# Kernel tuning notes

Measured on AMD Instinct MI355X. Metric: run time of the kernel, lower is better.

Reference implementation:

```python
import jax, jax.numpy as jnp
import numpy as np

N = 50000          # nodes
E = 800000         # edges (before self loops)
F_IN = 16
HID = 64
HEADS = 4
C = 64             # per-head out channels (concat=False)
G = 64             # graphs in batch
NEG_SLOPE = 0.2


def setup_inputs() -> dict:
    key = jax.random.key(0)
    ks = jax.random.split(key, 20)
    inp = {
        "x": jax.random.normal(ks[0], (N, F_IN), jnp.float32),
        "edge_index": jax.random.randint(ks[1], (2, E), 0, N, jnp.int64),
        "batch": jnp.sort(jax.random.randint(ks[2], (N,), 0, G, jnp.int64)),
        "W_in": jax.random.normal(ks[3], (HID, F_IN), jnp.float32) * 0.1,
        "b_in": jnp.zeros((HID,), jnp.float32),
        "W_out": jax.random.normal(ks[4], (1, HID), jnp.float32) * 0.1,
        "b_out": jnp.zeros((1,), jnp.float32),
    }
    for l in range(3):
        inp[f"W{l}"] = jax.random.normal(ks[5 + 4 * l], (HEADS * C, HID), jnp.float32) * 0.1
        inp[f"asrc{l}"] = jax.random.normal(ks[6 + 4 * l], (HEADS, C), jnp.float32) * 0.1
        inp[f"adst{l}"] = jax.random.normal(ks[7 + 4 * l], (HEADS, C), jnp.float32) * 0.1
        inp[f"bg{l}"] = jnp.zeros((HID,), jnp.float32)
    return inp


def _gat_layer(x, W, a_src, a_dst, bias, src, dst, n):
    # x: [N, HID] -> h: [N, HEADS, C]
    h = (x @ W.T).reshape(n, HEADS, C)
    alpha_s = jnp.einsum("nhc,hc->nh", h, a_src)   # [N, H]
    alpha_d = jnp.einsum("nhc,hc->nh", h, a_dst)
    e = jax.nn.leaky_relu(alpha_s[src] + alpha_d[dst], NEG_SLOPE)  # [E', H]
    # segment softmax over incoming edges of each dst node
    m = jax.ops.segment_max(e, dst, num_segments=n)
    e = jnp.exp(e - m[dst])
    s = jax.ops.segment_sum(e, dst, num_segments=n)
    alpha = e / (s[dst] + 1e-16)                                   # [E', H]
    msg = alpha[:, :, None] * h[src]                               # [E', H, C]
    out = jax.ops.segment_sum(msg, dst, num_segments=n)            # [N, H, C]
    return out.mean(axis=1) + bias                                 # concat=False: head mean


def reference(x, W_in, b_in, W0, asrc0, adst0, bg0, W1, asrc1, adst1, bg1,
              W2, asrc2, adst2, bg2, W_out, b_out, edge_index, batch):
    n = x.shape[0]
    # add self loops (PyG GATConv default)
    loops = jnp.arange(n, dtype=edge_index.dtype)
    src = jnp.concatenate([edge_index[0], loops])
    dst = jnp.concatenate([edge_index[1], loops])

    h = x @ W_in.T + b_in
    for W, a_s, a_d, bg in ((W0, asrc0, adst0, bg0),
                            (W1, asrc1, adst1, bg1),
                            (W2, asrc2, adst2, bg2)):
        h = jax.nn.relu(_gat_layer(h, W, a_s, a_d, bg, src, dst, n))
        # dropout p=0.2 is inactive in eval mode

    # global mean pool over graphs
    sums = jax.ops.segment_sum(h, batch, num_segments=G)
    cnt = jax.ops.segment_sum(jnp.ones((n,), h.dtype), batch, num_segments=G)
    graph_emb = sums / jnp.maximum(cnt, 1.0)[:, None]              # [G, HID]

    return jax.nn.sigmoid(graph_emb @ W_out.T + b_out)             # [G, 1]
```

## Files before the change

### kernel.cpp

```cpp
#include <hip/hip_runtime.h>
#include <hip/hip_bf16.h>
#include <hip/hip_fp16.h>

#define HID 64
#define HEADS 4
#define GCNT 64
#define F_IN 16
#define NEG 0.2f
#define NBUCK 256
#define BSLOT 6144
#define SCHUNK 2048

typedef _Float16 f16x8 __attribute__((ext_vector_type(8)));
typedef float f32x4 __attribute__((ext_vector_type(4)));

__device__ __forceinline__ unsigned pack_h2(float a, float b) {
  __half2 h = __floats2half2_rn(a, b);
  union { __half2 h; unsigned u; } c;
  c.h = h;
  return c.u;
}
__device__ __forceinline__ __half2 uas_h2(unsigned u) {
  union { unsigned u; __half2 h; } c;
  c.u = u;
  return c.h;
}
__device__ __forceinline__ unsigned h2_as_u(__half2 h) {
  union { __half2 h; unsigned u; } c;
  c.h = h;
  return c.u;
}
__device__ __forceinline__ __half2 xor16_add(__half2 v) {
  unsigned u = (unsigned)__shfl_xor((int)h2_as_u(v), 16, 64);
  return __hadd2(v, uas_h2(u));
}

__global__ __launch_bounds__(256) void k_pre(
    const float* __restrict__ W0, const float* __restrict__ asrc,
    const float* __restrict__ adst, int* __restrict__ bcur, float* __restrict__ va) {
  int t = threadIdx.x;
  if (blockIdx.x == 0) bcur[t] = 0;
  int idx = blockIdx.x * 256 + t;
  int q = idx >> 6, k = idx & 63;
  const float* a = (q < 4) ? asrc : adst;
  int h = q & 3;
  float s = 0.f;
  for (int c = 0; c < 64; ++c) s += a[h * 64 + c] * W0[(h * 64 + c) * 64 + k];
  va[idx] = s;
}

__global__ __launch_bounds__(256) void k_bucket(
    const int* __restrict__ ei, int* __restrict__ bcur,
    unsigned* __restrict__ tmp, int E, int N) {
  __shared__ int hist[NBUCK];
  __shared__ int base[NBUCK];
  int t = threadIdx.x;
  int start = blockIdx.x * SCHUNK;
  int end = min(start + SCHUNK, E + N);
  hist[t] = 0;
  __syncthreads();
  unsigned val[8];
  int rank[8];
  bool ok[8];
#pragma unroll
  for (int k = 0; k < 8; ++k) {
    int i = start + t + k * 256;
    ok[k] = i < end;
    if (ok[k]) {
      int s, d;
      if (i < E) {
        s = ei[i];
        d = ei[E + i];
      } else {
        s = d = i - E;
      }
      val[k] = ((unsigned)d << 16) | (unsigned)s;
      rank[k] = atomicAdd(&hist[d >> 8], 1);
    }
  }
  __syncthreads();
  int h = hist[t];
  base[t] = h ? atomicAdd(&bcur[t], h) : 0;
  __syncthreads();
#pragma unroll
  for (int k = 0; k < 8; ++k) {
    if (ok[k]) {
      int bk = (int)(val[k] >> 24);
      int idx = base[bk] + rank[k];
      if (idx < BSLOT) tmp[(size_t)bk * BSLOT + idx] = val[k];
    }
  }
}

__global__ __launch_bounds__(256) void k_bsort(
    const unsigned* __restrict__ tmp, const int* __restrict__ bcur,
    int* __restrict__ rowptr, int* __restrict__ col, int N) {
  __shared__ int s[NBUCK];
  __shared__ int hist[NBUCK];
  __shared__ int pref[NBUCK];
  int b = blockIdx.x, t = threadIdx.x;
  int c = min(bcur[t], BSLOT);
  s[t] = c;
  __syncthreads();
  for (int o = 1; o < 256; o <<= 1) {
    int x = (t >= o) ? s[t - o] : 0;
    __syncthreads();
    s[t] += x;
    __syncthreads();
  }
  int base = (b == 0) ? 0 : s[b - 1];
  int total = s[255];
  int cntb = min(bcur[b], BSLOT);
  hist[t] = 0;
  __syncthreads();
  for (int j = t; j < cntb; j += 256)
    atomicAdd(&hist[(tmp[(size_t)b * BSLOT + j] >> 16) & 255], 1);
  __syncthreads();
  int v = hist[t];
  pref[t] = v;
  __syncthreads();
  for (int o = 1; o < 256; o <<= 1) {
    int x = (t >= o) ? pref[t - o] : 0;
    __syncthreads();
    pref[t] += x;
    __syncthreads();
  }
  pref[t] -= v;
  __syncthreads();
  int node = b * 256 + t;
  if (node < N) rowptr[node] = base + pref[t];
  if (b == 255 && t == 255) rowptr[N] = total;
  hist[t] = 0;
  __syncthreads();
  for (int j = t; j < cntb; j += 256) {
    unsigned e = tmp[(size_t)b * BSLOT + j];
    int d8 = (int)((e >> 16) & 255);
    int r = atomicAdd(&hist[d8], 1);
    col[base + pref[d8] + r] = (int)(e & 0xffffu);
  }
}

__global__ void k_init(const float* __restrict__ x, const float* __restrict__ Win,
                       const float* __restrict__ bin,
                       const float* __restrict__ W0, const float* __restrict__ W1,
                       const float* __restrict__ W2,
                       __half* __restrict__ Wh3, __half* __restrict__ Wcat3,
                       float* __restrict__ sums, const float* __restrict__ va,
                       float* __restrict__ as_, float* __restrict__ ad_,
                       __half* __restrict__ hh, int N) {
  int b = blockIdx.x, t = threadIdx.x;
  if (b < 384) {
    int i = b * 256 + t;
    if (i < 49152) {
      const float* W = (i < 16384) ? W0 : (i < 32768) ? W1 : W2;
      Wh3[i] = __float2half(W[i & 16383]);
    } else {
      int j = i - 49152;
      int l = j >> 14;
      int r = j & 16383;
      int c = r >> 8;
      int k256 = r & 255;
      int h = k256 & 3, kk = k256 >> 2;
      const float* W = (l == 0) ? W0 : (l == 1) ? W1 : W2;
      Wcat3[j] = __float2half(0.25f * W[(h * 64 + c) * 64 + kk]);
    }
    return;
  }
  if (b < 401) {
    int i = (b - 384) * 256 + t;
    if (i < GCNT * HID + GCNT) sums[i] = 0.f;
    return;
  }
  int i = (b - 401) * 256 + t;
  if (i >= N * HID) return;
  int n = i >> 6, j = i & 63;
  const float* xr = x + (size_t)n * F_IN;
  const float* wr = Win + j * F_IN;
  float acc = bin[j];
#pragma unroll
  for (int k = 0; k < F_IN; ++k) acc += xr[k] * wr[k];
  hh[i] = __float2half(acc);
  float r[8];
#pragma unroll
  for (int q = 0; q < 8; ++q) {
    float v = acc * va[q * 64 + j];
#pragma unroll
    for (int o = 32; o; o >>= 1) v += __shfl_xor(v, o, 64);
    r[q] = v;
  }
  if (j == 0) {
    *(float4*)(as_ + (size_t)n * 4) = make_float4(r[0], r[1], r[2], r[3]);
    *(float4*)(ad_ + (size_t)n * 4) = make_float4(r[4], r[5], r[6], r[7]);
  }
}

__device__ __forceinline__ void gat_one_node(
    int node, int lane, const __half* __restrict__ h, const float* __restrict__ as_,
    const float* __restrict__ ad_, const int* __restrict__ rowptr,
    const int* __restrict__ col, __half* __restrict__ M, int N) {
  int r0 = rowptr[node];
  int deg = rowptr[node + 1] - r0;
  float4 adv = *(const float4*)(ad_ + (size_t)node * 4);

  if (deg <= 64) {
    int off = 0;
    float x0 = 0.f, x1 = 0.f, x2 = 0.f, x3 = 0.f;
    if (lane < deg) {
      int s = col[r0 + lane];
      off = s << 6;
      float4 av = *(const float4*)(as_ + (size_t)s * 4);
      float e0 = av.x + adv.x; e0 = (e0 > 0.f) ? e0 : NEG * e0;
      float e1 = av.y + adv.y; e1 = (e1 > 0.f) ? e1 : NEG * e1;
      float e2 = av.z + adv.z; e2 = (e2 > 0.f) ? e2 : NEG * e2;
      float e3 = av.w + adv.w; e3 = (e3 > 0.f) ? e3 : NEG * e3;
      x0 = __expf(fminf(e0, 60.f));
      x1 = __expf(fminf(e1, 60.f));
      x2 = __expf(fminf(e2, 60.f));
      x3 = __expf(fminf(e3, 60.f));
    }
    float s0 = x0, s1 = x1, s2 = x2, s3 = x3;
#pragma unroll
    for (int o = 32; o; o >>= 1) {
      s0 += __shfl_xor(s0, o, 64);
      s1 += __shfl_xor(s1, o, 64);
      s2 += __shfl_xor(s2, o, 64);
      s3 += __shfl_xor(s3, o, 64);
    }
    unsigned w01 = pack_h2(x0 / (s0 + 1e-16f), x1 / (s1 + 1e-16f));
    unsigned w23 = pack_h2(x2 / (s2 + 1e-16f), x3 / (s3 + 1e-16f));
    __half2 acc01 = __floats2half2_rn(0.f, 0.f);
    __half2 acc23 = acc01;
#pragma unroll 4
    for (int j = 0; j < deg; ++j) {
      int oj = __builtin_amdgcn_readlane(off, j) + lane;
      unsigned W01 = __builtin_amdgcn_readlane(w01, j);
      unsigned W23 = __builtin_amdgcn_readlane(w23, j);
      __half2 hv = __half2half2(h[oj]);
      acc01 = __hfma2(hv, uas_h2(W01), acc01);
      acc23 = __hfma2(hv, uas_h2(W23), acc23);
    }
    uint2 st;
    st.x = h2_as_u(acc01);
    st.y = h2_as_u(acc23);
    *(uint2*)&M[(size_t)node * 256 + lane * 4] = st;
    return;
  }
  float m0 = -1e30f, m1 = -1e30f, m2 = -1e30f, m3 = -1e30f;
  for (int j = lane; j < deg; j += 64) {
    int s = col[r0 + j];
    float4 av = *(const float4*)(as_ + (size_t)s * 4);
    float e0 = av.x + adv.x; e0 = (e0 > 0.f) ? e0 : NEG * e0; m0 = fmaxf(m0, e0);
    float e1 = av.y + adv.y; e1 = (e1 > 0.f) ? e1 : NEG * e1; m1 = fmaxf(m1, e1);
    float e2 = av.z + adv.z; e2 = (e2 > 0.f) ? e2 : NEG * e2; m2 = fmaxf(m2, e2);
    float e3 = av.w + adv.w; e3 = (e3 > 0.f) ? e3 : NEG * e3; m3 = fmaxf(m3, e3);
  }
#pragma unroll
  for (int o = 32; o; o >>= 1) {
    m0 = fmaxf(m0, __shfl_xor(m0, o, 64));
    m1 = fmaxf(m1, __shfl_xor(m1, o, 64));
    m2 = fmaxf(m2, __shfl_xor(m2, o, 64));
    m3 = fmaxf(m3, __shfl_xor(m3, o, 64));
  }
  float s0 = 0.f, s1 = 0.f, s2 = 0.f, s3 = 0.f;
  for (int j = lane; j < deg; j += 64) {
    int s = col[r0 + j];
    float4 av = *(const float4*)(as_ + (size_t)s * 4);
    float e0 = av.x + adv.x; e0 = (e0 > 0.f) ? e0 : NEG * e0; s0 += __expf(e0 - m0);
    float e1 = av.y + adv.y; e1 = (e1 > 0.f) ? e1 : NEG * e1; s1 += __expf(e1 - m1);
    float e2 = av.z + adv.z; e2 = (e2 > 0.f) ? e2 : NEG * e2; s2 += __expf(e2 - m2);
    float e3 = av.w + adv.w; e3 = (e3 > 0.f) ? e3 : NEG * e3; s3 += __expf(e3 - m3);
  }
#pragma unroll
  for (int o = 32; o; o >>= 1) {
    s0 += __shfl_xor(s0, o, 64);
    s1 += __shfl_xor(s1, o, 64);
    s2 += __shfl_xor(s2, o, 64);
    s3 += __shfl_xor(s3, o, 64);
  }
  float i0 = 1.f / (s0 + 1e-16f), i1 = 1.f / (s1 + 1e-16f);
  float i2 = 1.f / (s2 + 1e-16f), i3 = 1.f / (s3 + 1e-16f);
  float a0 = 0.f, a1 = 0.f, a2 = 0.f, a3 = 0.f;
  for (int j = 0; j < deg; ++j) {
    int s = col[r0 + j];
    float4 av = *(const float4*)(as_ + (size_t)s * 4);
    float e0 = av.x + adv.x; e0 = (e0 > 0.f) ? e0 : NEG * e0;
    float e1 = av.y + adv.y; e1 = (e1 > 0.f) ? e1 : NEG * e1;
    float e2 = av.z + adv.z; e2 = (e2 > 0.f) ? e2 : NEG * e2;
    float e3 = av.w + adv.w; e3 = (e3 > 0.f) ? e3 : NEG * e3;
    float hv = __half2float(h[(s << 6) + lane]);
    a0 = fmaf(__expf(e0 - m0) * i0, hv, a0);
    a1 = fmaf(__expf(e1 - m1) * i1, hv, a1);
    a2 = fmaf(__expf(e2 - m2) * i2, hv, a2);
    a3 = fmaf(__expf(e3 - m3) * i3, hv, a3);
  }
  uint2 st;
  st.x = pack_h2(a0, a1);
  st.y = pack_h2(a2, a3);
  *(uint2*)&M[(size_t)node * 256 + lane * 4] = st;
}

__global__ __launch_bounds__(256) void k_gat(
    const __half* __restrict__ h, const float* __restrict__ as_,
    const float* __restrict__ ad_, const int* __restrict__ rowptr,
    const int* __restrict__ col, __half* __restrict__ M, int N) {
  int lane = threadIdx.x & 63;
  int pr = (blockIdx.x << 2) | (threadIdx.x >> 6);
  int npairs = (N + 1) >> 1;
  if (pr >= npairs) return;
  int half = lane >> 5, l5 = lane & 31;

  int n0 = pr * 2;
  int n1 = min(n0 + 1, N - 1);
  int mynode = half ? n1 : n0;
  int r0 = rowptr[mynode];
  int dg = rowptr[mynode + 1] - r0;
  int dgA = __builtin_amdgcn_readlane(dg, 0);
  int dgB = __builtin_amdgcn_readlane(dg, 32);

  if (dgA <= 32 && dgB <= 32) {
    float4 adv = *(const float4*)(ad_ + (size_t)mynode * 4);
    int off = 0;
    float x0 = 0.f, x1 = 0.f, x2 = 0.f, x3 = 0.f;
    if (l5 < dg) {
      int s = col[r0 + l5];
      off = s << 6;
      float4 av = *(const float4*)(as_ + (size_t)s * 4);
      float e0 = av.x + adv.x; e0 = (e0 > 0.f) ? e0 : NEG * e0;
      float e1 = av.y + adv.y; e1 = (e1 > 0.f) ? e1 : NEG * e1;
      float e2 = av.z + adv.z; e2 = (e2 > 0.f) ? e2 : NEG * e2;
      float e3 = av.w + adv.w; e3 = (e3 > 0.f) ? e3 : NEG * e3;
      x0 = __expf(fminf(e0, 60.f));
      x1 = __expf(fminf(e1, 60.f));
      x2 = __expf(fminf(e2, 60.f));
      x3 = __expf(fminf(e3, 60.f));
    }
    float s0 = x0, s1 = x1, s2 = x2, s3 = x3;
#pragma unroll
    for (int o = 16; o; o >>= 1) {
      s0 += __shfl_xor(s0, o, 64);
      s1 += __shfl_xor(s1, o, 64);
      s2 += __shfl_xor(s2, o, 64);
      s3 += __shfl_xor(s3, o, 64);
    }
    unsigned w01 = pack_h2(x0 / (s0 + 1e-16f), x1 / (s1 + 1e-16f));
    unsigned w23 = pack_h2(x2 / (s2 + 1e-16f), x3 / (s3 + 1e-16f));

    int g = l5 >> 4, li = l5 & 15;
    const uint2* h4p = (const uint2*)h;
    __half2 z = __floats2half2_rn(0.f, 0.f);
    __half2 a0_01 = z, a0_23 = z, a1_01 = z, a1_23 = z;
    __half2 a2_01 = z, a2_23 = z, a3_01 = z, a3_23 = z;
    int mdeg = max(dgA, dgB);
    int baddr = half << 7;
#pragma unroll 2
    for (int j = 0; j < mdeg; j += 2) {
      int addr = baddr + (j + g) * 4;
      int oj = __builtin_amdgcn_ds_bpermute(addr, off);
      unsigned W01 = (unsigned)__builtin_amdgcn_ds_bpermute(addr, (int)w01);
      unsigned W23 = (unsigned)__builtin_amdgcn_ds_bpermute(addr, (int)w23);
      uint2 hv = h4p[(oj >> 2) + li];
      __half2 ha = uas_h2(hv.x), hb = uas_h2(hv.y);
      __half2 wA = uas_h2(W01), wB = uas_h2(W23);
      __half2 c0 = __low2half2(ha), c1 = __high2half2(ha);
      __half2 c2 = __low2half2(hb), c3 = __high2half2(hb);
      a0_01 = __hfma2(c0, wA, a0_01); a0_23 = __hfma2(c0, wB, a0_23);
      a1_01 = __hfma2(c1, wA, a1_01); a1_23 = __hfma2(c1, wB, a1_23);
      a2_01 = __hfma2(c2, wA, a2_01); a2_23 = __hfma2(c2, wB, a2_23);
      a3_01 = __hfma2(c3, wA, a3_01); a3_23 = __hfma2(c3, wB, a3_23);
    }
    a0_01 = xor16_add(a0_01); a0_23 = xor16_add(a0_23);
    a1_01 = xor16_add(a1_01); a1_23 = xor16_add(a1_23);
    a2_01 = xor16_add(a2_01); a2_23 = xor16_add(a2_23);
    a3_01 = xor16_add(a3_01); a3_23 = xor16_add(a3_23);
    if (g == 0) {
      size_t base = (size_t)mynode * 256 + li * 16;
      uint4 st1, st2;
      st1.x = h2_as_u(a0_01); st1.y = h2_as_u(a0_23);
      st1.z = h2_as_u(a1_01); st1.w = h2_as_u(a1_23);
      st2.x = h2_as_u(a2_01); st2.y = h2_as_u(a2_23);
      st2.z = h2_as_u(a3_01); st2.w = h2_as_u(a3_23);
      *(uint4*)&M[base] = st1;
      *(uint4*)&M[base + 8] = st2;
    }
  } else {
    gat_one_node(n0, lane, h, as_, ad_, rowptr, col, M, N);
    if (n1 != n0) gat_one_node(n1, lane, h, as_, ad_, rowptr, col, M, N);
  }
}

template <bool FIN>
__global__ __launch_bounds__(256) void k_fuse(
    const __half* __restrict__ M, const __half* __restrict__ Wcat,
    const float* __restrict__ bg, const __half* __restrict__ Wn,
    const float* __restrict__ asrc, const float* __restrict__ adst,
    __half* __restrict__ hh, float* __restrict__ as_, float* __restrict__ ad_,
    int N, int mtiles) {
  __shared__ __half lds[16 * 72];
  int lane = threadIdx.x & 63, wv = threadIdx.x >> 6;
  int quad = lane >> 4, n16 = lane & 15;
  const f16x8* MC = (const f16x8*)M;
  const f16x8* WC = (const f16x8*)Wcat;

  int ch1 = wv * 16 + n16;
  f16x8 b1[8];
#pragma unroll
  for (int i = 0; i < 8; ++i) b1[i] = WC[ch1 * 32 + i * 4 + quad];
  float bias1 = bg[ch1];

  f16x8 b2[4][2];
  float aw[4], dw[4];
  if (!FIN) {
    const f16x8* WN = (const f16x8*)Wn;
#pragma unroll
    for (int nt = 0; nt < 4; ++nt) {
      int ch = wv * 64 + nt * 16 + n16;
#pragma unroll
      for (int kh = 0; kh < 2; ++kh) b2[nt][kh] = WN[ch * 8 + kh * 4 + quad];
      aw[nt] = asrc[ch];
      dw[nt] = adst[ch];
    }
  }

  for (int mt = blockIdx.x; mt < mtiles; mt += gridDim.x) {
    __syncthreads();
    int m = mt * 16 + n16;
    if (m >= N) m = N - 1;
    f32x4 c1 = {0.f, 0.f, 0.f, 0.f};
#pragma unroll
    for (int i = 0; i < 8; ++i)
      c1 = __builtin_amdgcn_mfma_f32_16x16x32_f16(MC[m * 32 + i * 4 + quad], b1[i], c1, 0, 0, 0);
#pragma unroll
    for (int r = 0; r < 4; ++r) {
      float v = fmaxf(c1[r] + bias1, 0.f);
      lds[(quad * 4 + r) * 72 + ch1] = __float2half(v);
    }
    __syncthreads();
    {
      int t = threadIdx.x;
      int nd = t >> 4, c0 = (t & 15) * 4;
      int node = mt * 16 + nd;
      if (node < N) {
        uint2 v = *(const uint2*)&lds[nd * 72 + c0];
        *(uint2*)&hh[(size_t)node * 64 + c0] = v;
      }
    }
    if (!FIN) {
      f16x8 a0 = *(const f16x8*)&lds[n16 * 72 + quad * 8];
      f16x8 a1 = *(const f16x8*)&lds[n16 * 72 + 32 + quad * 8];
      f32x4 acc[4];
#pragma unroll
      for (int nt = 0; nt < 4; ++nt) {
        f32x4 z = {0.f, 0.f, 0.f, 0.f};
        z = __builtin_amdgcn_mfma_f32_16x16x32_f16(a0, b2[nt][0], z, 0, 0, 0);
        z = __builtin_amdgcn_mfma_f32_16x16x32_f16(a1, b2[nt][1], z, 0, 0, 0);
        acc[nt] = z;
      }
#pragma unroll
      for (int r = 0; r < 4; ++r) {
        float vs = 0.f, vd = 0.f;
#pragma unroll
        for (int nt = 0; nt < 4; ++nt) {
          vs = fmaf(acc[nt][r], aw[nt], vs);
          vd = fmaf(acc[nt][r], dw[nt], vd);
        }
#pragma unroll
        for (int o = 8; o; o >>= 1) {
          vs += __shfl_xor(vs, o, 64);
          vd += __shfl_xor(vd, o, 64);
        }
        int node = mt * 16 + quad * 4 + r;
        if (n16 == 0 && node < N) {
          as_[(size_t)node * 4 + wv] = vs;
          ad_[(size_t)node * 4 + wv] = vd;
        }
      }
    }
  }
}

__global__ __launch_bounds__(256) void k_pool(
    const __half* __restrict__ hh, const int* __restrict__ batch,
    float* __restrict__ sums, float* __restrict__ cnt, int N) {
  int c = threadIdx.x & 63, r = threadIdx.x >> 6;
  int base = blockIdx.x * 64 + r * 16;
  float acc = 0.f;
  int curg = -1, cacc = 0;
  for (int i = 0; i < 16; ++i) {
    int n = base + i;
    if (n >= N) break;
    int g = batch[n];
    if (g != curg) {
      if (curg >= 0) {
        atomicAdd(&sums[curg * HID + c], acc);
        if (c == 0) atomicAdd(&cnt[curg], (float)cacc);
      }
      curg = g; acc = 0.f; cacc = 0;
    }
    acc += __half2float(hh[(size_t)n * HID + c]);
    cacc++;
  }
  if (curg >= 0) {
    atomicAdd(&sums[curg * HID + c], acc);
    if (c == 0) atomicAdd(&cnt[curg], (float)cacc);
  }
}

__global__ void k_out(const float* __restrict__ sums, const float* __restrict__ cnt,
                      const float* __restrict__ Wout, const float* __restrict__ bout,
                      float* __restrict__ out) {
  int g = blockIdx.x, lane = threadIdx.x;
  float cg = fmaxf(cnt[g], 1.f);
  float v = (sums[g * HID + lane] / cg) * Wout[lane];
#pragma unroll
  for (int o = 32; o; o >>= 1) v += __shfl_xor(v, o, 64);
  if (lane == 0) out[g] = 1.f / (1.f + __expf(-v));
}

extern "C" void kernel_launch(void* const* d_in, const int* in_sizes, int n_in,
                              void* d_out, int out_size, void* d_ws, size_t ws_size,
                              hipStream_t stream) {
  const float* x    = (const float*)d_in[0];
  const int*   ei   = (const int*)d_in[1];
  const int*   batch= (const int*)d_in[2];
  const float* Win  = (const float*)d_in[3];
  const float* bin  = (const float*)d_in[4];
  const float* Wout = (const float*)d_in[5];
  const float* bout = (const float*)d_in[6];
  const float* Wl[3]    = {(const float*)d_in[7],  (const float*)d_in[11], (const float*)d_in[15]};
  const float* asrcl[3] = {(const float*)d_in[8],  (const float*)d_in[12], (const float*)d_in[16]};
  const float* adstl[3] = {(const float*)d_in[9],  (const float*)d_in[13], (const float*)d_in[17]};
  const float* bgl[3]   = {(const float*)d_in[10], (const float*)d_in[14], (const float*)d_in[18]};

  int N = in_sizes[2];
  int E = in_sizes[1] / 2;
  int EE = E + N;

  char* p = (char*)d_ws;
  auto alloc = [&](size_t bytes) {
    char* r = p;
    p += (bytes + 255) & ~(size_t)255;
    return r;
  };
  int*      rowptr = (int*)alloc((size_t)(N + 1) * 4);
  int*      col    = (int*)alloc((size_t)EE * 4);
  unsigned* tmp    = (unsigned*)alloc((size_t)NBUCK * BSLOT * 4);
  int*      bcur   = (int*)alloc(NBUCK * 4);
  float*    va     = (float*)alloc(8 * 64 * 4);
  __half*   hh     = (__half*)alloc((size_t)N * HID * 2);
  __half*   Mbuf   = (__half*)alloc((size_t)N * 256 * 2);
  float*    as_    = (float*)alloc((size_t)N * HEADS * 4);
  float*    ad_    = (float*)alloc((size_t)N * HEADS * 4);
  __half*   Wh3    = (__half*)alloc(3 * 16384 * 2);
  __half*   Wcat3  = (__half*)alloc(3 * 16384 * 2);
  float*    sums   = (float*)alloc((size_t)(GCNT * HID + GCNT) * 4);
  float*    cnt    = sums + GCNT * HID;

  int mtiles = (N + 15) / 16;
  int npairs = (N + 1) >> 1;

  k_pre<<<2, 256, 0, stream>>>(Wl[0], asrcl[0], adstl[0], bcur, va);
  k_bucket<<<(EE + SCHUNK - 1) / SCHUNK, 256, 0, stream>>>(ei, bcur, tmp, E, N);
  k_bsort<<<NBUCK, 256, 0, stream>>>(tmp, bcur, rowptr, col, N);

  k_init<<<401 + (N * HID + 255) / 256, 256, 0, stream>>>(
      x, Win, bin, Wl[0], Wl[1], Wl[2], Wh3, Wcat3, sums, va, as_, ad_, hh, N);

  k_gat<<<(npairs + 3) / 4, 256, 0, stream>>>(hh, as_, ad_, rowptr, col, Mbuf, N);
  for (int l = 0; l < 2; ++l) {
    k_fuse<false><<<1024, 256, 0, stream>>>(Mbuf, Wcat3 + l * 16384, bgl[l],
                                            Wh3 + (l + 1) * 16384, asrcl[l + 1], adstl[l + 1],
                                            hh, as_, ad_, N, mtiles);
    k_gat<<<(npairs + 3) / 4, 256, 0, stream>>>(hh, as_, ad_, rowptr, col, Mbuf, N);
  }
  k_fuse<true><<<1024, 256, 0, stream>>>(Mbuf, Wcat3 + 2 * 16384, bgl[2],
                                         nullptr, nullptr, nullptr,
                                         hh, as_, ad_, N, mtiles);

  k_pool<<<(N + 63) / 64, 256, 0, stream>>>(hh, batch, sums, cnt, N);
  k_out<<<GCNT, 64, 0, stream>>>(sums, cnt, Wout, bout, (float*)d_out);
}
```

Measured before the change: 346.8 us.

## Fuse GAT aggregation with projection kernel via shared-memory tile, ping-pong buffers

```diff
diff --git a/kernel.cpp b/kernel.cpp
--- a/kernel.cpp
+++ b/kernel.cpp
@@ -197,7 +197,7 @@
 __device__ __forceinline__ void gat_one_node(
     int node, int lane, const __half* __restrict__ h, const float* __restrict__ as_,
     const float* __restrict__ ad_, const int* __restrict__ rowptr,
-    const int* __restrict__ col, __half* __restrict__ M, int N) {
+    const int* __restrict__ col, __half* __restrict__ Mrow) {
   int r0 = rowptr[node];
   int deg = rowptr[node + 1] - r0;
   float4 adv = *(const float4*)(ad_ + (size_t)node * 4);
@@ -239,10 +239,8 @@
       acc01 = __hfma2(hv, uas_h2(W01), acc01);
       acc23 = __hfma2(hv, uas_h2(W23), acc23);
     }
-    uint2 st;
-    st.x = h2_as_u(acc01);
-    st.y = h2_as_u(acc23);
-    *(uint2*)&M[(size_t)node * 256 + lane * 4] = st;
+    *(__half2*)&Mrow[lane * 4] = acc01;
+    *(__half2*)&Mrow[lane * 4 + 2] = acc23;
     return;
   }
   float m0 = -1e30f, m1 = -1e30f, m2 = -1e30f, m3 = -1e30f;
@@ -293,186 +291,189 @@
     a2 = fmaf(__expf(e2 - m2) * i2, hv, a2);
     a3 = fmaf(__expf(e3 - m3) * i3, hv, a3);
   }
-  uint2 st;
-  st.x = pack_h2(a0, a1);
-  st.y = pack_h2(a2, a3);
-  *(uint2*)&M[(size_t)node * 256 + lane * 4] = st;
-}
-
-__global__ __launch_bounds__(256) void k_gat(
+  *(__half2*)&Mrow[lane * 4] = __floats2half2_rn(a0, a1);
+  *(__half2*)&Mrow[lane * 4 + 2] = __floats2half2_rn(a2, a3);
+}
+
+template <bool FIN>
+__global__ __launch_bounds__(256) void k_gatf(
     const __half* __restrict__ h, const float* __restrict__ as_,
     const float* __restrict__ ad_, const int* __restrict__ rowptr,
-    const int* __restrict__ col, __half* __restrict__ M, int N) {
-  int lane = threadIdx.x & 63;
-  int pr = (blockIdx.x << 2) | (threadIdx.x >> 6);
-  int npairs = (N + 1) >> 1;
-  if (pr >= npairs) return;
-  int half = lane >> 5, l5 = lane & 31;
-
-  int n0 = pr * 2;
-  int n1 = min(n0 + 1, N - 1);
-  int mynode = half ? n1 : n0;
-  int r0 = rowptr[mynode];
-  int dg = rowptr[mynode + 1] - r0;
-  int dgA = __builtin_amdgcn_readlane(dg, 0);
-  int dgB = __builtin_amdgcn_readlane(dg, 32);
-
-  if (dgA <= 32 && dgB <= 32) {
-    float4 adv = *(const float4*)(ad_ + (size_t)mynode * 4);
-    int off = 0;
-    float x0 = 0.f, x1 = 0.f, x2 = 0.f, x3 = 0.f;
-    if (l5 < dg) {
-      int s = col[r0 + l5];
-      off = s << 6;
-      float4 av = *(const float4*)(as_ + (size_t)s * 4);
-      float e0 = av.x + adv.x; e0 = (e0 > 0.f) ? e0 : NEG * e0;
-      float e1 = av.y + adv.y; e1 = (e1 > 0.f) ? e1 : NEG * e1;
-      float e2 = av.z + adv.z; e2 = (e2 > 0.f) ? e2 : NEG * e2;
-      float e3 = av.w + adv.w; e3 = (e3 > 0.f) ? e3 : NEG * e3;
-      x0 = __expf(fminf(e0, 60.f));
-      x1 = __expf(fminf(e1, 60.f));
-      x2 = __expf(fminf(e2, 60.f));
-      x3 = __expf(fminf(e3, 60.f));
-    }
-    float s0 = x0, s1 = x1, s2 = x2, s3 = x3;
-#pragma unroll
-    for (int o = 16; o; o >>= 1) {
-      s0 += __shfl_xor(s0, o, 64);
-      s1 += __shfl_xor(s1, o, 64);
-      s2 += __shfl_xor(s2, o, 64);
-      s3 += __shfl_xor(s3, o, 64);
-    }
-    unsigned w01 = pack_h2(x0 / (s0 + 1e-16f), x1 / (s1 + 1e-16f));
-    unsigned w23 = pack_h2(x2 / (s2 + 1e-16f), x3 / (s3 + 1e-16f));
-
-    int g = l5 >> 4, li = l5 & 15;
-    const uint2* h4p = (const uint2*)h;
-    __half2 z = __floats2half2_rn(0.f, 0.f);
-    __half2 a0_01 = z, a0_23 = z, a1_01 = z, a1_23 = z;
-    __half2 a2_01 = z, a2_23 = z, a3_01 = z, a3_23 = z;
-    int mdeg = max(dgA, dgB);
-    int baddr = half << 7;
-#pragma unroll 2
-    for (int j = 0; j < mdeg; j += 2) {
-      int addr = baddr + (j + g) * 4;
-      int oj = __builtin_amdgcn_ds_bpermute(addr, off);
-      unsigned W01 = (unsigned)__builtin_amdgcn_ds_bpermute(addr, (int)w01);
-      unsigned W23 = (unsigned)__builtin_amdgcn_ds_bpermute(addr, (int)w23);
-      uint2 hv = h4p[(oj >> 2) + li];
-      __half2 ha = uas_h2(hv.x), hb = uas_h2(hv.y);
-      __half2 wA = uas_h2(W01), wB = uas_h2(W23);
-      __half2 c0 = __low2half2(ha), c1 = __high2half2(ha);
-      __half2 c2 = __low2half2(hb), c3 = __high2half2(hb);
-      a0_01 = __hfma2(c0, wA, a0_01); a0_23 = __hfma2(c0, wB, a0_23);
-      a1_01 = __hfma2(c1, wA, a1_01); a1_23 = __hfma2(c1, wB, a1_23);
-      a2_01 = __hfma2(c2, wA, a2_01); a2_23 = __hfma2(c2, wB, a2_23);
-      a3_01 = __hfma2(c3, wA, a3_01); a3_23 = __hfma2(c3, wB, a3_23);
-    }
-    a0_01 = xor16_add(a0_01); a0_23 = xor16_add(a0_23);
-    a1_01 = xor16_add(a1_01); a1_23 = xor16_add(a1_23);
-    a2_01 = xor16_add(a2_01); a2_23 = xor16_add(a2_23);
-    a3_01 = xor16_add(a3_01); a3_23 = xor16_add(a3_23);
-    if (g == 0) {
-      size_t base = (size_t)mynode * 256 + li * 16;
-      uint4 st1, st2;
-      st1.x = h2_as_u(a0_01); st1.y = h2_as_u(a0_23);
-      st1.z = h2_as_u(a1_01); st1.w = h2_as_u(a1_23);
-      st2.x = h2_as_u(a2_01); st2.y = h2_as_u(a2_23);
-      st2.z = h2_as_u(a3_01); st2.w = h2_as_u(a3_23);
-      *(uint4*)&M[base] = st1;
-      *(uint4*)&M[base + 8] = st2;
-    }
-  } else {
-    gat_one_node(n0, lane, h, as_, ad_, rowptr, col, M, N);
-    if (n1 != n0) gat_one_node(n1, lane, h, as_, ad_, rowptr, col, M, N);
-  }
-}
-
-template <bool FIN>
-__global__ __launch_bounds__(256) void k_fuse(
-    const __half* __restrict__ M, const __half* __restrict__ Wcat,
+    const int* __restrict__ col, const __half* __restrict__ Wcat,
     const float* __restrict__ bg, const __half* __restrict__ Wn,
     const float* __restrict__ asrc, const float* __restrict__ adst,
-    __half* __restrict__ hh, float* __restrict__ as_, float* __restrict__ ad_,
-    int N, int mtiles) {
-  __shared__ __half lds[16 * 72];
-  int lane = threadIdx.x & 63, wv = threadIdx.x >> 6;
+    __half* __restrict__ hout, float* __restrict__ nas, float* __restrict__ nad,
+    int N) {
+  __shared__ __half Mt[16 * 264];
+  __shared__ __half O[16 * 72];
+  int tid = threadIdx.x;
+  int lane = tid & 63, wv = tid >> 6;
+  int tile = blockIdx.x;
+  int half = lane >> 5, l5 = lane & 31;
+  int npairs = (N + 1) >> 1;
+
+  for (int pp = 0; pp < 2; ++pp) {
+    int pr = tile * 8 + wv * 2 + pp;
+    if (pr >= npairs) break;
+    int n0 = pr * 2;
+    int n1 = min(n0 + 1, N - 1);
+    int mynode = half ? n1 : n0;
+    int r0 = rowptr[mynode];
+    int dg = rowptr[mynode + 1] - r0;
+    int dgA = __builtin_amdgcn_readlane(dg, 0);
+    int dgB = __builtin_amdgcn_readlane(dg, 32);
+
+    if (dgA <= 32 && dgB <= 32) {
+      float4 adv = *(const float4*)(ad_ + (size_t)mynode * 4);
+      int off = 0;
+      float x0 = 0.f, x1 = 0.f, x2 = 0.f, x3 = 0.f;
+      if (l5 < dg) {
+        int s = col[r0 + l5];
+        off = s << 6;
+        float4 av = *(const float4*)(as_ + (size_t)s * 4);
+        float e0 = av.x + adv.x; e0 = (e0 > 0.f) ? e0 : NEG * e0;
+        float e1 = av.y + adv.y; e1 = (e1 > 0.f) ? e1 : NEG * e1;
+        float e2 = av.z + adv.z; e2 = (e2 > 0.f) ? e2 : NEG * e2;
+        float e3 = av.w + adv.w; e3 = (e3 > 0.f) ? e3 : NEG * e3;
+        x0 = __expf(fminf(e0, 60.f));
+        x1 = __expf(fminf(e1, 60.f));
+        x2 = __expf(fminf(e2, 60.f));
+        x3 = __expf(fminf(e3, 60.f));
+      }
+      float s0 = x0, s1 = x1, s2 = x2, s3 = x3;
+#pragma unroll
+      for (int o = 16; o; o >>= 1) {
+        s0 += __shfl_xor(s0, o, 64);
+        s1 += __shfl_xor(s1, o, 64);
+        s2 += __shfl_xor(s2, o, 64);
+        s3 += __shfl_xor(s3, o, 64);
+      }
+      unsigned w01 = pack_h2(x0 / (s0 + 1e-16f), x1 / (s1 + 1e-16f));
+      unsigned w23 = pack_h2(x2 / (s2 + 1e-16f), x3 / (s3 + 1e-16f));
+
+      int g = l5 >> 4, li = l5 & 15;
+      const uint2* h4p = (const uint2*)h;
+      __half2 z = __floats2half2_rn(0.f, 0.f);
+      __half2 a0_01 = z, a0_23 = z, a1_01 = z, a1_23 = z;
+      __half2 a2_01 = z, a2_23 = z, a3_01 = z, a3_23 = z;
+      int mdeg = max(dgA, dgB);
+      int baddr = half << 7;
+#pragma unroll 2
+      for (int j = 0; j < mdeg; j += 2) {
+        int addr = baddr + (j + g) * 4;
+        int oj = __builtin_amdgcn_ds_bpermute(addr, off);
+        unsigned W01 = (unsigned)__builtin_amdgcn_ds_bpermute(addr, (int)w01);
+        unsigned W23 = (unsigned)__builtin_amdgcn_ds_bpermute(addr, (int)w23);
+        uint2 hv = h4p[(oj >> 2) + li];
+        __half2 ha = uas_h2(hv.x), hb = uas_h2(hv.y);
+        __half2 wA = uas_h2(W01), wB = uas_h2(W23);
+        __half2 c0 = __low2half2(ha), c1 = __high2half2(ha);
+        __half2 c2 = __low2half2(hb), c3 = __high2half2(hb);
+        a0_01 = __hfma2(c0, wA, a0_01); a0_23 = __hfma2(c0, wB, a0_23);
+        a1_01 = __hfma2(c1, wA, a1_01); a1_23 = __hfma2(c1, wB, a1_23);
+        a2_01 = __hfma2(c2, wA, a2_01); a2_23 = __hfma2(c2, wB, a2_23);
+        a3_01 = __hfma2(c3, wA, a3_01); a3_23 = __hfma2(c3, wB, a3_23);
+      }
+      a0_01 = xor16_add(a0_01); a0_23 = xor16_add(a0_23);
+      a1_01 = xor16_add(a1_01); a1_23 = xor16_add(a1_23);
+      a2_01 = xor16_add(a2_01); a2_23 = xor16_add(a2_23);
+      a3_01 = xor16_add(a3_01); a3_23 = xor16_add(a3_23);
+      if (g == 0) {
+        __half* row = &Mt[(mynode & 15) * 264 + li * 16];
+        uint4 st1, st2;
+        st1.x = h2_as_u(a0_01); st1.y = h2_as_u(a0_23);
+        st1.z = h2_as_u(a1_01); st1.w = h2_as_u(a1_23);
+        st2.x = h2_as_u(a2_01); st2.y = h2_as_u(a2_23);
+        st2.z = h2_as_u(a3_01); st2.w = h2_as_u(a3_23);
+        *(uint4*)&row[0] = st1;
+        *(uint4*)&row[8] = st2;
+      }
+    } else {
+      gat_one_node(n0, lane, h, as_, ad_, rowptr, col, &Mt[(n0 & 15) * 264]);
+      if (n1 != n0) gat_one_node(n1, lane, h, as_, ad_, rowptr, col, &Mt[(n1 & 15) * 264]);
+    }
+  }
+  __syncthreads();
+
   int quad = lane >> 4, n16 = lane & 15;
-  const f16x8* MC = (const f16x8*)M;
   const f16x8* WC = (const f16x8*)Wcat;
-
   int ch1 = wv * 16 + n16;
-  f16x8 b1[8];
-#pragma unroll
-  for (int i = 0; i < 8; ++i) b1[i] = WC[ch1 * 32 + i * 4 + quad];
   float bias1 = bg[ch1];
-
-  f16x8 b2[4][2];
-  float aw[4], dw[4];
+  f32x4 c1 = {0.f, 0.f, 0.f, 0.f};
+#pragma unroll
+  for (int i = 0; i < 8; ++i) {
+    f16x8 a = *(const f16x8*)&Mt[n16 * 264 + (i * 4 + quad) * 8];
+    c1 = __builtin_amdgcn_mfma_f32_16x16x32_f16(a, WC[ch1 * 32 + i * 4 + quad], c1, 0, 0, 0);
+  }
+#pragma unroll
+  for (int r = 0; r < 4; ++r) {
+    float v = fmaxf(c1[r] + bias1, 0.f);
+    O[(quad * 4 + r) * 72 + ch1] = __float2half(v);
+  }
+  __syncthreads();
+  {
+    int nd = tid >> 4, c0 = (tid & 15) * 4;
+    int node = tile * 16 + nd;
+    if (node < N) {
+      uint2 v = *(const uint2*)&O[nd * 72 + c0];
+      *(uint2*)&hout[(size_t)node * 64 + c0] = v;
+    }
+  }
   if (!FIN) {
     const f16x8* WN = (const f16x8*)Wn;
+    f16x8 a0 = *(const f16x8*)&O[n16 * 72 + quad * 8];
+    f16x8 a1 = *(const f16x8*)&O[n16 * 72 + 32 + quad * 8];
 #pragma unroll
     for (int nt = 0; nt < 4; ++nt) {
       int ch = wv * 64 + nt * 16 + n16;
-#pragma unroll
-      for (int kh = 0; kh < 2; ++kh) b2[nt][kh] = WN[ch * 8 + kh * 4 + quad];
-      aw[nt] = asrc[ch];
-      dw[nt] = adst[ch];
-    }
-  }
-
-  for (int mt = blockIdx.x; mt < mtiles; mt += gridDim.x) {
-    __syncthreads();
-    int m = mt * 16 + n16;
-    if (m >= N) m = N - 1;
-    f32x4 c1 = {0.f, 0.f, 0.f, 0.f};
-#pragma unroll
-    for (int i = 0; i < 8; ++i)
-      c1 = __builtin_amdgcn_mfma_f32_16x16x32_f16(MC[m * 32 + i * 4 + quad], b1[i], c1, 0, 0, 0);
+      f32x4 zz = {0.f, 0.f, 0.f, 0.f};
+      zz = __builtin_amdgcn_mfma_f32_16x16x32_f16(a0, WN[ch * 8 + quad], zz, 0, 0, 0);
+      zz = __builtin_amdgcn_mfma_f32_16x16x32_f16(a1, WN[ch * 8 + 4 + quad], zz, 0, 0, 0);
+      float aw = asrc[ch], dw = adst[ch];
+      if (nt == 0) {
+#pragma unroll
+        for (int r = 0; r < 4; ++r) { c1[r] = zz[r] * aw; }
+      } else {
+#pragma unroll
+        for (int r = 0; r < 4; ++r) { c1[r] = fmaf(zz[r], aw, c1[r]); }
+      }
+      if (nt == 0) {
+#pragma unroll
+        for (int r = 0; r < 4; ++r) {  }
+      }
+      static_assert(true, "");
+      if (nt == 0) {
+      }
+      (void)dw;
+      break;
+    }
+    f32x4 accs[4];
+#pragma unroll
+    for (int nt = 0; nt < 4; ++nt) {
+      int ch = wv * 64 + nt * 16 + n16;
+      f32x4 zz = {0.f, 0.f, 0.f, 0.f};
+      zz = __builtin_amdgcn_mfma_f32_16x16x32_f16(a0, WN[ch * 8 + quad], zz, 0, 0, 0);
+      zz = __builtin_amdgcn_mfma_f32_16x16x32_f16(a1, WN[ch * 8 + 4 + quad], zz, 0, 0, 0);
+      accs[nt] = zz;
+    }
 #pragma unroll
     for (int r = 0; r < 4; ++r) {
-      float v = fmaxf(c1[r] + bias1, 0.f);
-      lds[(quad * 4 + r) * 72 + ch1] = __float2half(v);
-    }
-    __syncthreads();
-    {
-      int t = threadIdx.x;
-      int nd = t >> 4, c0 = (t & 15) * 4;
-      int node = mt * 16 + nd;
-      if (node < N) {
-        uint2 v = *(const uint2*)&lds[nd * 72 + c0];
-        *(uint2*)&hh[(size_t)node * 64 + c0] = v;
-      }
-    }
-    if (!FIN) {
-      f16x8 a0 = *(const f16x8*)&lds[n16 * 72 + quad * 8];
-      f16x8 a1 = *(const f16x8*)&lds[n16 * 72 + 32 + quad * 8];
-      f32x4 acc[4];
+      float vs = 0.f, vd = 0.f;
 #pragma unroll
       for (int nt = 0; nt < 4; ++nt) {
-        f32x4 z = {0.f, 0.f, 0.f, 0.f};
-        z = __builtin_amdgcn_mfma_f32_16x16x32_f16(a0, b2[nt][0], z, 0, 0, 0);
-        z = __builtin_amdgcn_mfma_f32_16x16x32_f16(a1, b2[nt][1], z, 0, 0, 0);
-        acc[nt] = z;
-      }
-#pragma unroll
-      for (int r = 0; r < 4; ++r) {
-        float vs = 0.f, vd = 0.f;
-#pragma unroll
-        for (int nt = 0; nt < 4; ++nt) {
-          vs = fmaf(acc[nt][r], aw[nt], vs);
-          vd = fmaf(acc[nt][r], dw[nt], vd);
-        }
-#pragma unroll
-        for (int o = 8; o; o >>= 1) {
-          vs += __shfl_xor(vs, o, 64);
-          vd += __shfl_xor(vd, o, 64);
-        }
-        int node = mt * 16 + quad * 4 + r;
-        if (n16 == 0 && node < N) {
-          as_[(size_t)node * 4 + wv] = vs;
-          ad_[(size_t)node * 4 + wv] = vd;
-        }
+        int ch = wv * 64 + nt * 16 + n16;
+        vs = fmaf(accs[nt][r], asrc[ch], vs);
+        vd = fmaf(accs[nt][r], adst[ch], vd);
+      }
+#pragma unroll
+      for (int o = 8; o; o >>= 1) {
+        vs += __shfl_xor(vs, o, 64);
+        vd += __shfl_xor(vd, o, 64);
+      }
+      int node = tile * 16 + quad * 4 + r;
+      if (n16 == 0 && node < N) {
+        nas[(size_t)node * 4 + wv] = vs;
+        nad[(size_t)node * 4 + wv] = vd;
       }
     }
   }
@@ -546,36 +547,36 @@
   unsigned* tmp    = (unsigned*)alloc((size_t)NBUCK * BSLOT * 4);
   int*      bcur   = (int*)alloc(NBUCK * 4);
   float*    va     = (float*)alloc(8 * 64 * 4);
-  __half*   hh     = (__half*)alloc((size_t)N * HID * 2);
-  __half*   Mbuf   = (__half*)alloc((size_t)N * 256 * 2);
-  float*    as_    = (float*)alloc((size_t)N * HEADS * 4);
-  float*    ad_    = (float*)alloc((size_t)N * HEADS * 4);
+  __half*   hhA    = (__half*)alloc((size_t)N * HID * 2);
+  __half*   hhB    = (__half*)alloc((size_t)N * HID * 2);
+  float*    asA    = (float*)alloc((size_t)N * HEADS * 4);
+  float*    adA    = (float*)alloc((size_t)N * HEADS * 4);
+  float*    asB    = (float*)alloc((size_t)N * HEADS * 4);
+  float*    adB    = (float*)alloc((size_t)N * HEADS * 4);
   __half*   Wh3    = (__half*)alloc(3 * 16384 * 2);
   __half*   Wcat3  = (__half*)alloc(3 * 16384 * 2);
   float*    sums   = (float*)alloc((size_t)(GCNT * HID + GCNT) * 4);
   float*    cnt    = sums + GCNT * HID;
 
-  int mtiles = (N + 15) / 16;
-  int npairs = (N + 1) >> 1;
+  int tiles = (N + 15) / 16;
 
   k_pre<<<2, 256, 0, stream>>>(Wl[0], asrcl[0], adstl[0], bcur, va);
   k_bucket<<<(EE + SCHUNK - 1) / SCHUNK, 256, 0, stream>>>(ei, bcur, tmp, E, N);
   k_bsort<<<NBUCK, 256, 0, stream>>>(tmp, bcur, rowptr, col, N);
 
   k_init<<<401 + (N * HID + 255) / 256, 256, 0, stream>>>(
-      x, Win, bin, Wl[0], Wl[1], Wl[2], Wh3, Wcat3, sums, va, as_, ad_, hh, N);
-
-  k_gat<<<(npairs + 3) / 4, 256, 0, stream>>>(hh, as_, ad_, rowptr, col, Mbuf, N);
-  for (int l = 0; l < 2; ++l) {
-    k_fuse<false><<<1024, 256, 0, stream>>>(Mbuf, Wcat3 + l * 16384, bgl[l],
-                                            Wh3 + (l + 1) * 16384, asrcl[l + 1], adstl[l + 1],
-                                            hh, as_, ad_, N, mtiles);
-    k_gat<<<(npairs + 3) / 4, 256, 0, stream>>>(hh, as_, ad_, rowptr, col, Mbuf, N);
-  }
-  k_fuse<true><<<1024, 256, 0, stream>>>(Mbuf, Wcat3 + 2 * 16384, bgl[2],
-                                         nullptr, nullptr, nullptr,
-                                         hh, as_, ad_, N, mtiles);
-
-  k_pool<<<(N + 63) / 64, 256, 0, stream>>>(hh, batch, sums, cnt, N);
+      x, Win, bin, Wl[0], Wl[1], Wl[2], Wh3, Wcat3, sums, va, asA, adA, hhA, N);
+
+  k_gatf<false><<<tiles, 256, 0, stream>>>(hhA, asA, adA, rowptr, col,
+                                           Wcat3, bgl[0], Wh3 + 16384, asrcl[1], adstl[1],
+                                           hhB, asB, adB, N);
+  k_gatf<false><<<tiles, 256, 0, stream>>>(hhB, asB, adB, rowptr, col,
+                                           Wcat3 + 16384, bgl[1], Wh3 + 32768, asrcl[2], adstl[2],
+                                           hhA, asA, adA, N);
+  k_gatf<true><<<tiles, 256, 0, stream>>>(hhA, asA, adA, rowptr, col,
+                                          Wcat3 + 32768, bgl[2], nullptr, nullptr, nullptr,
+                                          hhB, nullptr, nullptr, N);
+
+  k_pool<<<(N + 63) / 64, 256, 0, stream>>>(hhB, batch, sums, cnt, N);
   k_out<<<GCNT, 64, 0, stream>>>(sums, cnt, Wout, bout, (float*)d_out);
 }
```

Measured after the change: 338.6 us. 2.4% less time.
